# Kernel optimization log

Hardware: AMD Instinct MI355X
Metric: run time of the kernel (lower is better)

Reference implementation:

```python
import jax, jax.numpy as jnp
import numpy as np
from jax import lax

NUM_CLASSES = 80
TOPK = 13
ALPHA = 1.0
BETA = 6.0
EPS = 1e-9
P = 150000
N = 256


def _make_boxes(key, n, scale):
    k1, k2 = jax.random.split(key)
    xy = jax.random.uniform(k1, (n, 2), dtype=jnp.float32) * scale
    wh = jax.random.uniform(k2, (n, 2), dtype=jnp.float32) * (0.2 * scale) + 1.0
    return jnp.concatenate([xy, xy + wh], axis=-1)  # valid x1y1x2y2


def setup_inputs() -> dict:
    key = jax.random.key(0)
    k1, k2, k3, k4 = jax.random.split(key, 4)
    cls_pred = jax.random.uniform(k1, (P, NUM_CLASSES), dtype=jnp.float32)
    bbox_pred = _make_boxes(k2, P, 640.0)
    bbox_gt = _make_boxes(k3, N, 640.0)
    # FG labels are > 0 (code indexes cls_pred[label-1])
    label_gt = jax.random.randint(k4, (N, 1), 1, NUM_CLASSES + 1, dtype=jnp.int32)
    return {"cls_pred": cls_pred, "bbox_pred": bbox_pred, "label_gt": label_gt, "bbox_gt": bbox_gt}


def _ious(bbox1, bbox2, eps=EPS):
    # bbox1: (N,4) gt, bbox2: (P,4) pred -> (N,P)
    b1 = bbox1[:, None, :]
    b2 = bbox2[None, :, :]
    x1y1 = jnp.maximum(b1[..., 0:2], b2[..., 0:2])
    x2y2 = jnp.minimum(b1[..., 2:4], b2[..., 2:4])
    inter = jnp.clip(x2y2 - x1y1, 0.0).prod(-1)
    area1 = jnp.clip(b1[..., 2:4] - b1[..., 0:2], 0.0).prod(-1)
    area2 = jnp.clip(b2[..., 2:4] - b2[..., 0:2], 0.0).prod(-1)
    return inter / (area1 + area2 - inter + eps)


def _metrics_topk(metrics, topk, eps=EPS):
    n, num_priors = metrics.shape
    topk_vals, topk_idxs = lax.top_k(metrics, topk)  # (N,k)
    keep = topk_vals.max(axis=-1, keepdims=True) > eps
    topk_idxs = jnp.where(keep, topk_idxs, 0)
    rows = jnp.arange(n)[:, None]
    counts = jnp.zeros((n, num_priors), jnp.int32).at[rows, topk_idxs].add(1)
    is_in_topk = jnp.where(counts > 1, 0, counts)
    return is_in_topk.astype(metrics.dtype)


def reference(cls_pred, bbox_pred, label_gt, bbox_gt):
    num_priors, num_classes = cls_pred.shape
    n_gt = bbox_gt.shape[0]
    ious = _ious(bbox_gt, bbox_pred)  # (N,P)
    lbl = label_gt.reshape(-1).astype(jnp.int32)  # (N,)
    bbox_cls_scores = jnp.take(cls_pred.T, lbl - 1, axis=0)  # (N,P)
    alignment_metrics = jnp.power(bbox_cls_scores, ALPHA) * jnp.power(ious, BETA)
    mask_positive = _metrics_topk(alignment_metrics, TOPK)  # (N,P) float 0/1
    mask_positive_sum = mask_positive.sum(axis=0)  # (P,)
    # conflict resolution: priors claimed by >1 gt go to the max-iou gt.
    # Applying unconditionally equals the torch data-dependent branch.
    is_max_iou = (jnp.arange(n_gt)[:, None] == ious.argmax(axis=0)[None, :]).astype(ious.dtype)
    mask_positive = jnp.where(mask_positive_sum[None, :] > 1, is_max_iou, mask_positive)
    mask_positive_sum = mask_positive.sum(axis=0)
    assigned_gt_index = mask_positive.argmax(axis=0)  # (P,)
    assigned_labels = lbl[assigned_gt_index]  # (P,)
    assigned_cls = jax.nn.one_hot(assigned_labels - 1, num_classes, dtype=jnp.int32)
    assigned_bboxes = bbox_gt[assigned_gt_index]  # (P,4)
    assigned_labels = jnp.where(mask_positive_sum > 0, assigned_labels, 0)
    return (assigned_gt_index, assigned_labels, assigned_cls, assigned_bboxes)
```

## Files before the change

kernel.cpp:

```cpp
#include <hip/hip_runtime.h>

#define TOPK 13
#define NCLS 80
#define EPSF 1e-9f
#define NSEG 32
#define GPB  8
#define CAP3 512
#define MCAP (64 * TOPK)

__global__ __launch_bounds__(256) void setup(const int* __restrict__ lbl,
                                             int* __restrict__ count,
                                             int* __restrict__ firstg,
                                             int* __restrict__ gorder, int P, int N) {
    int t = threadIdx.x;
    if (blockIdx.x == 0) {
        __shared__ int key[256];
        key[t] = (t < N) ? ((lbl[t] << 8) | t) : 0x7FFFFFFF;
        __syncthreads();
        for (int k = 2; k <= 256; k <<= 1) {
            for (int j = k >> 1; j >= 1; j >>= 1) {
                int ixj = t ^ j;
                if (ixj > t) {
                    int a = key[t], b = key[ixj];
                    bool up = ((t & k) == 0);
                    if (up ? (a > b) : (a < b)) { key[t] = b; key[ixj] = a; }
                }
                __syncthreads();
            }
        }
        if (t < N) gorder[t] = key[t] & 0xFF;
    } else {
        int base = (blockIdx.x - 1) * 1024 + t * 4;
        if (base + 3 < P) {
            *(int4*)&count[base]  = make_int4(0, 0, 0, 0);
            *(int4*)&firstg[base] = make_int4(0x7FFFFFFF, 0x7FFFFFFF, 0x7FFFFFFF, 0x7FFFFFFF);
        } else {
            for (int i = base; i < P; i++) { count[i] = 0; firstg[i] = 0x7FFFFFFF; }
        }
    }
}

__global__ __launch_bounds__(512, 6) void phaseA1(const float* __restrict__ cls,
                                                  const float4* __restrict__ bboxp,
                                                  const float4* __restrict__ bboxg,
                                                  const int* __restrict__ lbl,
                                                  const int* __restrict__ gorder,
                                                  float2* __restrict__ cand,
                                                  int P, int N, int seglen) {
#pragma clang fp contract(off)
    const int s = blockIdx.x, tile = blockIdx.y, t = threadIdx.x;
    const int wv = t >> 6, lane = t & 63;
    const int pstart = s * seglen;
    int pend = pstart + seglen; if (pend > P) pend = P;

    __shared__ float2 mbuf[GPB][MCAP];
    __shared__ int ctr[GPB];
    int* pbuf = (int*)&mbuf[0][0];

    float4 gb[GPB];
#pragma unroll
    for (int j = 0; j < GPB; j++) {
        int gi8 = tile * GPB + j;
        int gj = (gi8 < N) ? gorder[gi8] : -1;
        gb[j] = (gj >= 0) ? bboxg[gj] : make_float4(0.f, 0.f, 0.f, 0.f);
    }
    if (t < GPB) ctr[t] = 0;
    __syncthreads();

    auto testapp = [&](float4 pb, int p, bool force) {
#pragma unroll
        for (int j = 0; j < GPB; j++) {
            float dx = fminf(gb[j].z, pb.z) - fmaxf(gb[j].x, pb.x);
            float dy = fminf(gb[j].w, pb.w) - fmaxf(gb[j].y, pb.y);
            bool want = ((dx > 0.0f) && (dy > 0.0f)) || force;
            if (want) {
                int slot = atomicAdd(&ctr[j], 1);
                if (slot < CAP3) pbuf[j * CAP3 + slot] = p;
            }
        }
    };

    int p = pstart + t;
    if (p < pend) { testapp(bboxp[p], p, t < 16); p += 512; }
    for (; p + 1536 < pend; p += 2048) {
        float4 pb0 = bboxp[p];
        float4 pb1 = bboxp[p + 512];
        float4 pb2 = bboxp[p + 1024];
        float4 pb3 = bboxp[p + 1536];
        testapp(pb0, p, false);
        testapp(pb1, p + 512, false);
        testapp(pb2, p + 1024, false);
        testapp(pb3, p + 1536, false);
    }
    for (; p < pend; p += 512) testapp(bboxp[p], p, false);
    __syncthreads();

    const int gi8 = tile * GPB + wv;
    const bool myValid = gi8 < N;
    const int gj = myValid ? gorder[gi8] : 0;
    const float4 gbw = bboxg[gj];
    const float gaw = fmaxf(gbw.z - gbw.x, 0.0f) * fmaxf(gbw.w - gbw.y, 0.0f);
    const int cidx = lbl[gj] - 1;
    const int rawtotal = ctr[wv];

    float v[TOPK]; int id[TOPK];
#pragma unroll
    for (int k = 0; k < TOPK; k++) { v[k] = -1.0f; id[k] = 0x7FFFFFFF; }

    auto ins = [&](float m, int pp) {
        bool b12 = (m > v[TOPK - 1]) || (m == v[TOPK - 1] && pp < id[TOPK - 1]);
        if (b12) {
#pragma unroll
            for (int k = TOPK - 1; k >= 1; k--) {
                bool a = (m > v[k - 1]) || (m == v[k - 1] && pp < id[k - 1]);
                bool b = (m > v[k]) || (m == v[k] && pp < id[k]);
                float nv = a ? v[k - 1] : (b ? m : v[k]);
                int   ni = a ? id[k - 1] : (b ? pp : id[k]);
                v[k] = nv; id[k] = ni;
            }
            bool a0 = (m > v[0]) || (m == v[0] && pp < id[0]);
            if (a0) { v[0] = m; id[0] = pp; }
        }
    };

    auto evalm = [&](float4 pb, float sc) -> float {
        float pa = fmaxf(pb.z - pb.x, 0.0f) * fmaxf(pb.w - pb.y, 0.0f);
        float xx1 = fmaxf(gbw.x, pb.x), yy1 = fmaxf(gbw.y, pb.y);
        float xx2 = fminf(gbw.z, pb.z), yy2 = fminf(gbw.w, pb.w);
        float inter = fmaxf(xx2 - xx1, 0.0f) * fmaxf(yy2 - yy1, 0.0f);
        float iou = inter / (((gaw + pa) - inter) + EPSF);
        float i2 = iou * iou;
        return sc * ((i2 * i2) * i2);
    };

    if (rawtotal <= CAP3) {
        int e = lane;
        for (; e + 64 < rawtotal; e += 128) {
            int pp0 = pbuf[wv * CAP3 + e];
            int pp1 = pbuf[wv * CAP3 + e + 64];
            float4 pb0 = bboxp[pp0];
            float4 pb1 = bboxp[pp1];
            float sc0 = cls[(size_t)pp0 * NCLS + cidx];
            float sc1 = cls[(size_t)pp1 * NCLS + cidx];
            float m0 = evalm(pb0, sc0);
            float m1 = evalm(pb1, sc1);
            ins(m0, pp0);
            ins(m1, pp1);
        }
        for (; e < rawtotal; e += 64) {
            int pp = pbuf[wv * CAP3 + e];
            float4 pb = bboxp[pp];
            float sc = cls[(size_t)pp * NCLS + cidx];
            ins(evalm(pb, sc), pp);
        }
    } else if (myValid) {
        for (int pp = pstart + lane; pp < pend; pp += 64) {
            float4 pb = bboxp[pp];
            float sc = cls[(size_t)pp * NCLS + cidx];
            ins(evalm(pb, sc), pp);
        }
    }
    __syncthreads();

    float2* wl = mbuf[wv];
#pragma unroll
    for (int k = 0; k < TOPK; k++)
        wl[lane * TOPK + k] = make_float2(v[k], __int_as_float(id[k]));
    __syncthreads();
    for (int str = 32; str >= 1; str >>= 1) {
        if (lane < str) {
            float2 merged[TOPK];
            int a = 0, b = 0;
            const int ba = lane * TOPK, bb = (lane + str) * TOPK;
#pragma unroll
            for (int k = 0; k < TOPK; k++) {
                float2 fa = wl[ba + a], fb = wl[bb + b];
                int ia = __float_as_int(fa.y), ib = __float_as_int(fb.y);
                bool takeA = (fa.x > fb.x) || (fa.x == fb.x && ia < ib);
                merged[k] = takeA ? fa : fb;
                a += takeA; b += !takeA;
            }
#pragma unroll
            for (int k = 0; k < TOPK; k++) wl[ba + k] = merged[k];
        }
        __syncthreads();
    }
    if (lane < TOPK && myValid)
        cand[((size_t)gj * NSEG + s) * TOPK + lane] = wl[lane];
}

__global__ __launch_bounds__(512) void phaseA2(const float2* __restrict__ cand,
                                               int* __restrict__ count,
                                               int* __restrict__ firstg) {
    const int g = blockIdx.x;
    const int t = threadIdx.x;
    const int M = NSEG * TOPK;
    __shared__ float cv[512];
    __shared__ int   ci[512];
    if (t < M) {
        float2 e = cand[(size_t)g * M + t];
        cv[t] = e.x; ci[t] = __float_as_int(e.y);
    } else {
        cv[t] = -1.0f; ci[t] = 0x7FFFFFFF;
    }
    __syncthreads();
    for (int k = 2; k <= 512; k <<= 1) {
        for (int j = k >> 1; j >= 1; j >>= 1) {
            int ixj = t ^ j;
            if (ixj > t) {
                float va = cv[t], vb = cv[ixj];
                int   ia = ci[t], ib = ci[ixj];
                bool aBeforeB = (va > vb) || (va == vb && ia < ib);
                bool dirFwd = ((t & k) == 0);
                bool doswap = dirFwd ? !aBeforeB : aBeforeB;
                if (doswap) { cv[t] = vb; ci[t] = ib; cv[ixj] = va; ci[ixj] = ia; }
            }
            __syncthreads();
        }
    }
    if (t < TOPK && cv[0] > EPSF) {
        int pi = ci[t];
        atomicAdd(&count[pi], 1);
        atomicMin(&firstg[pi], g);
    }
}

__global__ __launch_bounds__(256) void phaseCF(const float4* __restrict__ bboxp,
                                               const float4* __restrict__ bboxg,
                                               const int* __restrict__ lbl,
                                               const int* __restrict__ count,
                                               const int* __restrict__ firstg,
                                               float* __restrict__ out0,
                                               float* __restrict__ out1,
                                               float4* __restrict__ outcls4,
                                               float4* __restrict__ outbox4, int P, int N) {
#pragma clang fp contract(off)
    __shared__ float4 gbS[256];
    __shared__ int glS[256];
    __shared__ int clsl[256];
    int t = threadIdx.x;
    if (t < N) { gbS[t] = bboxg[t]; glS[t] = lbl[t]; }
    __syncthreads();
    int p0 = blockIdx.x * 256;
    int nloc = P - p0; if (nloc > 256) nloc = 256;
    if (t < nloc) {
        int p = p0 + t;
        int cnt = count[p];
        int gi = 0, pos = 0;
        if (cnt == 1) { gi = firstg[p]; pos = 1; }
        else if (cnt > 1) {
            float4 pb = bboxp[p];
            float pa = fmaxf(pb.z - pb.x, 0.0f) * fmaxf(pb.w - pb.y, 0.0f);
            float best = -1.0f;
            for (int g = 0; g < N; g++) {
                float4 g4 = gbS[g];
                float gar = fmaxf(g4.z - g4.x, 0.0f) * fmaxf(g4.w - g4.y, 0.0f);
                float xx1 = fmaxf(g4.x, pb.x), yy1 = fmaxf(g4.y, pb.y);
                float xx2 = fminf(g4.z, pb.z), yy2 = fminf(g4.w, pb.w);
                float inter = fmaxf(xx2 - xx1, 0.0f) * fmaxf(yy2 - yy1, 0.0f);
                float iou = inter / (((gar + pa) - inter) + EPSF);
                if (iou > best) { best = iou; gi = g; }
            }
            pos = 1;
        }
        out0[p] = (float)gi;
        out1[p] = pos ? (float)glS[gi] : 0.0f;
        clsl[t] = glS[gi] - 1;
        outbox4[p] = gbS[gi];
    }
    __syncthreads();
    for (int f = t; f < nloc * 20; f += 256) {
        int pl = f / 20, q = f - pl * 20;
        int cl = clsl[pl], c0 = q * 4;
        float4 vv = make_float4(c0 == cl ? 1.0f : 0.0f, c0 + 1 == cl ? 1.0f : 0.0f,
                                c0 + 2 == cl ? 1.0f : 0.0f, c0 + 3 == cl ? 1.0f : 0.0f);
        outcls4[(size_t)p0 * 20 + f] = vv;
    }
}

__global__ __launch_bounds__(256) void phaseC1(const float4* __restrict__ bboxp,
                                               const float4* __restrict__ bboxg,
                                               const int* __restrict__ lbl,
                                               const int* __restrict__ count,
                                               const int* __restrict__ firstg,
                                               float* __restrict__ out0,
                                               float* __restrict__ out1, int P, int N) {
#pragma clang fp contract(off)
    __shared__ float4 gbS[256];
    __shared__ int glS[256];
    if (threadIdx.x < (unsigned)N) {
        gbS[threadIdx.x] = bboxg[threadIdx.x];
        glS[threadIdx.x] = lbl[threadIdx.x];
    }
    __syncthreads();
    int p = blockIdx.x * 256 + threadIdx.x;
    if (p >= P) return;
    int cnt = count[p];
    int gi = 0, pos = 0;
    if (cnt == 1) { gi = firstg[p]; pos = 1; }
    else if (cnt > 1) {
        float4 pb = bboxp[p];
        float pa = fmaxf(pb.z - pb.x, 0.0f) * fmaxf(pb.w - pb.y, 0.0f);
        float best = -1.0f;
        for (int g = 0; g < N; g++) {
            float4 g4 = gbS[g];
            float gar = fmaxf(g4.z - g4.x, 0.0f) * fmaxf(g4.w - g4.y, 0.0f);
            float xx1 = fmaxf(g4.x, pb.x), yy1 = fmaxf(g4.y, pb.y);
            float xx2 = fminf(g4.z, pb.z), yy2 = fminf(g4.w, pb.w);
            float inter = fmaxf(xx2 - xx1, 0.0f) * fmaxf(yy2 - yy1, 0.0f);
            float iou = inter / (((gar + pa) - inter) + EPSF);
            if (iou > best) { best = iou; gi = g; }
        }
        pos = 1;
    }
    out0[p] = (float)gi;
    out1[p] = pos ? (float)glS[gi] : 0.0f;
}

__global__ __launch_bounds__(256) void phaseC2(const float4* __restrict__ bboxg,
                                               const int* __restrict__ lbl,
                                               const float* __restrict__ out0,
                                               float* __restrict__ outcls,
                                               float* __restrict__ outbox, int P, int N) {
    __shared__ float gbb[256 * 4];
    __shared__ int glS[256];
    __shared__ int clsl[256];
    __shared__ int gil[256];
    int tid = threadIdx.x;
    if (tid < N) {
        float4 b = bboxg[tid];
        gbb[tid * 4 + 0] = b.x; gbb[tid * 4 + 1] = b.y;
        gbb[tid * 4 + 2] = b.z; gbb[tid * 4 + 3] = b.w;
        glS[tid] = lbl[tid];
    }
    __syncthreads();
    int p0 = blockIdx.x * 256;
    int nloc = P - p0; if (nloc > 256) nloc = 256;
    if (tid < nloc) {
        int gi = (int)out0[p0 + tid];
        gil[tid] = gi;
        clsl[tid] = glS[gi] - 1;
    }
    __syncthreads();
    for (int f = tid; f < nloc * NCLS; f += 256) {
        int pl = f / NCLS;
        int c  = f - pl * NCLS;
        outcls[(size_t)p0 * NCLS + f] = (c == clsl[pl]) ? 1.0f : 0.0f;
    }
    for (int f = tid; f < nloc * 4; f += 256) {
        int pl = f >> 2, k = f & 3;
        outbox[(size_t)p0 * 4 + f] = gbb[gil[pl] * 4 + k];
    }
}

extern "C" void kernel_launch(void* const* d_in, const int* in_sizes, int n_in,
                              void* d_out, int out_size, void* d_ws, size_t ws_size,
                              hipStream_t stream) {
    const float* cls_pred  = (const float*)d_in[0];
    const float* bbox_pred = (const float*)d_in[1];
    const int*   label_gt  = (const int*)d_in[2];
    const float* bbox_gt   = (const float*)d_in[3];
    int P = in_sizes[1] / 4;
    int N = in_sizes[3] / 4;

    float* out    = (float*)d_out;
    float* out0   = out;
    float* out1   = out + (size_t)P;
    float* outcls = out + (size_t)2 * P;
    float* outbox = out + (size_t)82 * P;

    int pb = (P + 255) / 256;
    int seglen = (P + NSEG - 1) / NSEG;
    int gtiles = (N + GPB - 1) / GPB;
    dim3 gridA1(NSEG, gtiles);
    int setupBlocks = 1 + (P + 1023) / 1024;
    size_t candBytes = (size_t)N * NSEG * TOPK * sizeof(float2);
    size_t needWs = (size_t)P * 8 + candBytes + (size_t)N * 4 + 64;

    if (ws_size >= needWs) {
        int*    count  = (int*)d_ws;
        int*    firstg = count + P;
        float2* cand   = (float2*)(firstg + P);
        int*    gorder = (int*)((char*)cand + candBytes);

        setup<<<setupBlocks, 256, 0, stream>>>(label_gt, count, firstg, gorder, P, N);
        phaseA1<<<gridA1, 512, 0, stream>>>(cls_pred, (const float4*)bbox_pred,
                                            (const float4*)bbox_gt, label_gt, gorder,
                                            cand, P, N, seglen);
        phaseA2<<<N, 512, 0, stream>>>(cand, count, firstg);
        phaseCF<<<pb, 256, 0, stream>>>((const float4*)bbox_pred, (const float4*)bbox_gt,
                                        label_gt, count, firstg, out0, out1,
                                        (float4*)outcls, (float4*)outbox, P, N);
    } else {
        int*    count  = (int*)outbox;
        int*    firstg = ((int*)outbox) + P;
        float2* cand   = (float2*)outcls;
        int*    gorder = (int*)((char*)cand + candBytes);

        setup<<<setupBlocks, 256, 0, stream>>>(label_gt, count, firstg, gorder, P, N);
        phaseA1<<<gridA1, 512, 0, stream>>>(cls_pred, (const float4*)bbox_pred,
                                            (const float4*)bbox_gt, label_gt, gorder,
                                            cand, P, N, seglen);
        phaseC1<<<pb, 256, 0, stream>>>((const float4*)bbox_pred, (const float4*)bbox_gt,
                                        label_gt, count, firstg, out0, out1, P, N);
        phaseC2<<<pb, 256, 0, stream>>>((const float4*)bbox_gt, label_gt, out0,
                                        outcls, outbox, P, N);
    }
}
```

Before: 215.4 us.

## Pack top-k entries into 64-bit keys and merge with wave shuffles

Packs each (metric, prior index) pair into a single order-preserving 64-bit key, so every insertion and compare becomes one integer comparison instead of a float-plus-index tie-break. The per-wave top-13 merge that went through shared memory with block-wide barriers is replaced by a register-resident bitonic merge over 16 slots using xor shuffles. The shared merge buffer is dropped, which cuts LDS use and lets launch bounds request 8 waves per SIMD instead of 6. PhaseA2's bitonic sort uses the same keys. The risks are more register pressure from 16 u64 slots, and a small extra cost from doing each 64-bit shuffle as two 32-bit shuffles.

```diff
diff --git a/kernel.cpp b/kernel.cpp
--- a/kernel.cpp
+++ b/kernel.cpp
@@ -6,7 +6,14 @@
 #define NSEG 32
 #define GPB  8
 #define CAP3 512
-#define MCAP (64 * TOPK)
+
+typedef unsigned long long u64;
+
+__device__ __forceinline__ u64 shfl_xor64(u64 x, int m) {
+    int lo = __shfl_xor((int)(unsigned)(x & 0xFFFFFFFFull), m, 64);
+    int hi = __shfl_xor((int)(unsigned)(x >> 32), m, 64);
+    return ((u64)(unsigned)hi << 32) | (unsigned)lo;
+}
 
 __global__ __launch_bounds__(256) void setup(const int* __restrict__ lbl,
                                              int* __restrict__ count,
@@ -40,12 +47,12 @@
     }
 }
 
-__global__ __launch_bounds__(512, 6) void phaseA1(const float* __restrict__ cls,
+__global__ __launch_bounds__(512, 8) void phaseA1(const float* __restrict__ cls,
                                                   const float4* __restrict__ bboxp,
                                                   const float4* __restrict__ bboxg,
                                                   const int* __restrict__ lbl,
                                                   const int* __restrict__ gorder,
-                                                  float2* __restrict__ cand,
+                                                  u64* __restrict__ cand,
                                                   int P, int N, int seglen) {
 #pragma clang fp contract(off)
     const int s = blockIdx.x, tile = blockIdx.y, t = threadIdx.x;
@@ -53,9 +60,8 @@
     const int pstart = s * seglen;
     int pend = pstart + seglen; if (pend > P) pend = P;
 
-    __shared__ float2 mbuf[GPB][MCAP];
+    __shared__ int pbuf[GPB][CAP3];
     __shared__ int ctr[GPB];
-    int* pbuf = (int*)&mbuf[0][0];
 
     float4 gb[GPB];
 #pragma unroll
@@ -75,7 +81,7 @@
             bool want = ((dx > 0.0f) && (dy > 0.0f)) || force;
             if (want) {
                 int slot = atomicAdd(&ctr[j], 1);
-                if (slot < CAP3) pbuf[j * CAP3 + slot] = p;
+                if (slot < CAP3) pbuf[j][slot] = p;
             }
         }
     };
@@ -103,123 +109,116 @@
     const int cidx = lbl[gj] - 1;
     const int rawtotal = ctr[wv];
 
-    float v[TOPK]; int id[TOPK];
-#pragma unroll
-    for (int k = 0; k < TOPK; k++) { v[k] = -1.0f; id[k] = 0x7FFFFFFF; }
-
-    auto ins = [&](float m, int pp) {
-        bool b12 = (m > v[TOPK - 1]) || (m == v[TOPK - 1] && pp < id[TOPK - 1]);
-        if (b12) {
+    u64 K[16];
+#pragma unroll
+    for (int k = 0; k < 16; k++) K[k] = 0ull;
+
+    auto ins = [&](u64 key) {
+        if (key > K[TOPK - 1]) {
 #pragma unroll
             for (int k = TOPK - 1; k >= 1; k--) {
-                bool a = (m > v[k - 1]) || (m == v[k - 1] && pp < id[k - 1]);
-                bool b = (m > v[k]) || (m == v[k] && pp < id[k]);
-                float nv = a ? v[k - 1] : (b ? m : v[k]);
-                int   ni = a ? id[k - 1] : (b ? pp : id[k]);
-                v[k] = nv; id[k] = ni;
-            }
-            bool a0 = (m > v[0]) || (m == v[0] && pp < id[0]);
-            if (a0) { v[0] = m; id[0] = pp; }
+                bool a = key > K[k - 1];
+                K[k] = a ? K[k - 1] : (key > K[k] ? key : K[k]);
+            }
+            if (key > K[0]) K[0] = key;
         }
     };
 
-    auto evalm = [&](float4 pb, float sc) -> float {
+    auto evalk = [&](float4 pb, float sc, int pp) -> u64 {
         float pa = fmaxf(pb.z - pb.x, 0.0f) * fmaxf(pb.w - pb.y, 0.0f);
         float xx1 = fmaxf(gbw.x, pb.x), yy1 = fmaxf(gbw.y, pb.y);
         float xx2 = fminf(gbw.z, pb.z), yy2 = fminf(gbw.w, pb.w);
         float inter = fmaxf(xx2 - xx1, 0.0f) * fmaxf(yy2 - yy1, 0.0f);
         float iou = inter / (((gaw + pa) - inter) + EPSF);
         float i2 = iou * iou;
-        return sc * ((i2 * i2) * i2);
+        float m = sc * ((i2 * i2) * i2);
+        unsigned ub = __float_as_uint(m);
+        ub ^= ((unsigned)((int)ub >> 31)) | 0x80000000u;
+        return ((u64)ub << 32) | (unsigned)(0x7FFFFFFF - pp);
     };
 
     if (rawtotal <= CAP3) {
         int e = lane;
         for (; e + 64 < rawtotal; e += 128) {
-            int pp0 = pbuf[wv * CAP3 + e];
-            int pp1 = pbuf[wv * CAP3 + e + 64];
+            int pp0 = pbuf[wv][e];
+            int pp1 = pbuf[wv][e + 64];
             float4 pb0 = bboxp[pp0];
             float4 pb1 = bboxp[pp1];
             float sc0 = cls[(size_t)pp0 * NCLS + cidx];
             float sc1 = cls[(size_t)pp1 * NCLS + cidx];
-            float m0 = evalm(pb0, sc0);
-            float m1 = evalm(pb1, sc1);
-            ins(m0, pp0);
-            ins(m1, pp1);
+            u64 k0 = evalk(pb0, sc0, pp0);
+            u64 k1 = evalk(pb1, sc1, pp1);
+            ins(k0);
+            ins(k1);
         }
         for (; e < rawtotal; e += 64) {
-            int pp = pbuf[wv * CAP3 + e];
+            int pp = pbuf[wv][e];
             float4 pb = bboxp[pp];
             float sc = cls[(size_t)pp * NCLS + cidx];
-            ins(evalm(pb, sc), pp);
+            ins(evalk(pb, sc, pp));
         }
     } else if (myValid) {
         for (int pp = pstart + lane; pp < pend; pp += 64) {
             float4 pb = bboxp[pp];
             float sc = cls[(size_t)pp * NCLS + cidx];
-            ins(evalm(pb, sc), pp);
-        }
-    }
-    __syncthreads();
-
-    float2* wl = mbuf[wv];
-#pragma unroll
-    for (int k = 0; k < TOPK; k++)
-        wl[lane * TOPK + k] = make_float2(v[k], __int_as_float(id[k]));
-    __syncthreads();
-    for (int str = 32; str >= 1; str >>= 1) {
-        if (lane < str) {
-            float2 merged[TOPK];
-            int a = 0, b = 0;
-            const int ba = lane * TOPK, bb = (lane + str) * TOPK;
-#pragma unroll
-            for (int k = 0; k < TOPK; k++) {
-                float2 fa = wl[ba + a], fb = wl[bb + b];
-                int ia = __float_as_int(fa.y), ib = __float_as_int(fb.y);
-                bool takeA = (fa.x > fb.x) || (fa.x == fb.x && ia < ib);
-                merged[k] = takeA ? fa : fb;
-                a += takeA; b += !takeA;
-            }
-#pragma unroll
-            for (int k = 0; k < TOPK; k++) wl[ba + k] = merged[k];
-        }
-        __syncthreads();
-    }
+            ins(evalk(pb, sc, pp));
+        }
+    }
+
+    for (int str = 1; str < 64; str <<= 1) {
+#pragma unroll
+        for (int i = 0; i < 8; i++) {
+            u64 pa = shfl_xor64(K[15 - i], str);
+            u64 pb = shfl_xor64(K[i], str);
+            u64 a = K[i], b = K[15 - i];
+            K[i]      = (a > pa) ? a : pa;
+            K[15 - i] = (b > pb) ? b : pb;
+        }
+#pragma unroll
+        for (int j = 8; j >= 1; j >>= 1) {
+#pragma unroll
+            for (int i = 0; i < 16; i++) {
+                if ((i & j) == 0) {
+                    u64 a = K[i], b = K[i | j];
+                    u64 mx = (a > b) ? a : b;
+                    u64 mn = (a > b) ? b : a;
+                    K[i] = mx; K[i | j] = mn;
+                }
+            }
+        }
+    }
+
+    u64 outk = 0ull;
+#pragma unroll
+    for (int k = 0; k < TOPK; k++) outk = (lane == k) ? K[k] : outk;
     if (lane < TOPK && myValid)
-        cand[((size_t)gj * NSEG + s) * TOPK + lane] = wl[lane];
-}
-
-__global__ __launch_bounds__(512) void phaseA2(const float2* __restrict__ cand,
+        cand[((size_t)gj * NSEG + s) * TOPK + lane] = outk;
+}
+
+__global__ __launch_bounds__(512) void phaseA2(const u64* __restrict__ cand,
                                                int* __restrict__ count,
                                                int* __restrict__ firstg) {
     const int g = blockIdx.x;
     const int t = threadIdx.x;
     const int M = NSEG * TOPK;
-    __shared__ float cv[512];
-    __shared__ int   ci[512];
-    if (t < M) {
-        float2 e = cand[(size_t)g * M + t];
-        cv[t] = e.x; ci[t] = __float_as_int(e.y);
-    } else {
-        cv[t] = -1.0f; ci[t] = 0x7FFFFFFF;
-    }
+    __shared__ u64 kv[512];
+    kv[t] = (t < M) ? cand[(size_t)g * M + t] : 0ull;
     __syncthreads();
     for (int k = 2; k <= 512; k <<= 1) {
         for (int j = k >> 1; j >= 1; j >>= 1) {
             int ixj = t ^ j;
             if (ixj > t) {
-                float va = cv[t], vb = cv[ixj];
-                int   ia = ci[t], ib = ci[ixj];
-                bool aBeforeB = (va > vb) || (va == vb && ia < ib);
+                u64 a = kv[t], b = kv[ixj];
                 bool dirFwd = ((t & k) == 0);
-                bool doswap = dirFwd ? !aBeforeB : aBeforeB;
-                if (doswap) { cv[t] = vb; ci[t] = ib; cv[ixj] = va; ci[ixj] = ia; }
+                bool doswap = dirFwd ? (a < b) : (a > b);
+                if (doswap) { kv[t] = b; kv[ixj] = a; }
             }
             __syncthreads();
         }
     }
-    if (t < TOPK && cv[0] > EPSF) {
-        int pi = ci[t];
+    const unsigned encEpsHi = __float_as_uint(EPSF) | 0x80000000u;
+    if (t < TOPK && (unsigned)(kv[0] >> 32) > encEpsHi) {
+        int pi = 0x7FFFFFFF - (int)(unsigned)(kv[t] & 0xFFFFFFFFull);
         atomicAdd(&count[pi], 1);
         atomicMin(&firstg[pi], g);
     }
@@ -374,14 +373,14 @@
     int gtiles = (N + GPB - 1) / GPB;
     dim3 gridA1(NSEG, gtiles);
     int setupBlocks = 1 + (P + 1023) / 1024;
-    size_t candBytes = (size_t)N * NSEG * TOPK * sizeof(float2);
+    size_t candBytes = (size_t)N * NSEG * TOPK * sizeof(u64);
     size_t needWs = (size_t)P * 8 + candBytes + (size_t)N * 4 + 64;
 
     if (ws_size >= needWs) {
-        int*    count  = (int*)d_ws;
-        int*    firstg = count + P;
-        float2* cand   = (float2*)(firstg + P);
-        int*    gorder = (int*)((char*)cand + candBytes);
+        int* count  = (int*)d_ws;
+        int* firstg = count + P;
+        u64* cand   = (u64*)(firstg + P);
+        int* gorder = (int*)((char*)cand + candBytes);
 
         setup<<<setupBlocks, 256, 0, stream>>>(label_gt, count, firstg, gorder, P, N);
         phaseA1<<<gridA1, 512, 0, stream>>>(cls_pred, (const float4*)bbox_pred,
@@ -392,10 +391,10 @@
                                         label_gt, count, firstg, out0, out1,
                                         (float4*)outcls, (float4*)outbox, P, N);
     } else {
-        int*    count  = (int*)outbox;
-        int*    firstg = ((int*)outbox) + P;
-        float2* cand   = (float2*)outcls;
-        int*    gorder = (int*)((char*)cand + candBytes);
+        int* count  = (int*)outbox;
+        int* firstg = ((int*)outbox) + P;
+        u64* cand   = (u64*)outcls;
+        int* gorder = (int*)((char*)cand + candBytes);
 
         setup<<<setupBlocks, 256, 0, stream>>>(label_gt, count, firstg, gorder, P, N);
         phaseA1<<<gridA1, 512, 0, stream>>>(cls_pred, (const float4*)bbox_pred,
```

After: 204.8 us. -5.0%, faster.
